# Optimization experiments

Hardware: AMD Instinct MI355X
Metric: run time of the kernel (lower is better)

Reference implementation:

```python
import jax, jax.numpy as jnp
import numpy as np

EPS = 1e-5
H = 6  # num_heads

def batchnorm(x, g, b):
    # BatchNorm1d over node dim using batch statistics (biased var, eps=1e-5)
    mu = x.mean(0)
    var = jnp.mean((x - mu) ** 2, 0)
    return (x - mu) * jax.lax.rsqrt(var + EPS) * g + b

def setup_inputs() -> dict:
    key = jax.random.key(0)
    ks = jax.random.split(key, 16)
    N, E, D = 20000, 200000, 384
    DH = 2 * D  # mlp hidden = dim * mlp_ratio(2.0)
    s = 0.05
    lin = lambda k, i, o: jax.random.normal(k, (i, o), jnp.float32) * s
    inp = {}
    inp['x'] = jax.random.normal(ks[0], (N, D), jnp.float32)
    inp['edge_index'] = jax.random.randint(ks[1], (2, E), 0, N)
    inp['edge_attr'] = jax.random.normal(ks[2], (E, D), jnp.float32)
    # norm1
    inp['g1'] = jnp.ones((D,), jnp.float32); inp['b1'] = jnp.zeros((D,), jnp.float32)
    # TransformerConv-style attention (concat=True, beta=False, edge_dim=D)
    inp['Wq'] = lin(ks[3], D, D); inp['bq'] = jnp.zeros((D,), jnp.float32)
    inp['Wk'] = lin(ks[4], D, D); inp['bk'] = jnp.zeros((D,), jnp.float32)
    inp['Wv'] = lin(ks[5], D, D); inp['bv'] = jnp.zeros((D,), jnp.float32)
    inp['We'] = lin(ks[6], D, D)  # lin_edge, no bias
    inp['Wskip'] = lin(ks[7], D, D); inp['bskip'] = jnp.zeros((D,), jnp.float32)
    # norm2
    inp['g2'] = jnp.ones((D,), jnp.float32); inp['b2'] = jnp.zeros((D,), jnp.float32)
    # Mlp
    inp['W1'] = lin(ks[8], D, DH); inp['bm1'] = jnp.zeros((DH,), jnp.float32)
    inp['W2'] = lin(ks[9], DH, D); inp['bm2'] = jnp.zeros((D,), jnp.float32)
    return inp

def reference(x, edge_index, edge_attr, g1, b1, Wq, bq, Wk, bk, Wv, bv, We, Wskip, bskip, g2, b2, W1, bm1, W2, bm2):
    N, D = x.shape
    Dh = D // H
    scale = 1.0 / jnp.sqrt(jnp.float32(Dh))
    h = batchnorm(x, g1, b1)
    q = (h @ Wq + bq).reshape(N, H, Dh)
    k = (h @ Wk + bk).reshape(N, H, Dh)
    v = (h @ Wv + bv).reshape(N, H, Dh)
    e = (edge_attr @ We).reshape(-1, H, Dh)  # [E,H,Dh]
    src, dst = edge_index[0], edge_index[1]
    ke = k[src] + e  # edge attr added to key
    ve = v[src] + e  # and to value (PyG TransformerConv)
    logits = jnp.einsum('ehd,ehd->eh', q[dst], ke) * scale  # [E,H]
    # segment softmax over incoming edges of each dst node
    m = jax.ops.segment_max(logits, dst, num_segments=N)
    a = jnp.exp(logits - m[dst])
    ssum = jax.ops.segment_sum(a, dst, num_segments=N)
    denom = ssum[dst]
    a = a / jnp.where(denom == 0, 1.0, denom)
    agg = jax.ops.segment_sum(a[:, :, None] * ve, dst, num_segments=N).reshape(N, D)
    attn = agg + (h @ Wskip + bskip)  # root skip (lin_skip)
    x = x + attn  # residual 1 (drop_path/dropout disabled in eval)
    h2 = batchnorm(x, g2, b2)
    mlp = jax.nn.gelu(h2 @ W1 + bm1, approximate=False) @ W2 + bm2
    return x + mlp
```

## Files before the change

### kernel.cpp

```cpp
#include <hip/hip_runtime.h>
#include <hip/hip_bf16.h>

#define DD 384
#define NH 6
#define DHID 768

typedef __attribute__((ext_vector_type(8))) short bf16x8;
typedef __attribute__((ext_vector_type(4))) float f32x4;

__device__ __forceinline__ void gload_lds16(const void* gsrc, void* ldst) {
  __builtin_amdgcn_global_load_lds((const __attribute__((address_space(1))) void*)gsrc,
                                   (__attribute__((address_space(3))) void*)ldst,
                                   16, 0, 0);
}

__global__ __launch_bounds__(384) void bn_stats_k(const float* __restrict__ x, float* __restrict__ sums,
                                                  float* __restrict__ sq, int N, int rpb) {
  int d = threadIdx.x;
  int r0 = blockIdx.x * rpb;
  int r1 = min(r0 + rpb, N);
  float s = 0.f, ss = 0.f;
  for (int r = r0; r < r1; ++r) {
    float v = x[(size_t)r * DD + d];
    s += v; ss += v * v;
  }
  atomicAdd(&sums[d], s);
  atomicAdd(&sq[d], ss);
}

__global__ void bn_finalize_k(const float* sums, const float* sq, const float* g, const float* b,
                              float* a, float* c, int N) {
  int d = blockIdx.x * blockDim.x + threadIdx.x;
  if (d >= DD) return;
  float inv = 1.f / (float)N;
  float mu = sums[d] * inv;
  float var = sq[d] * inv - mu * mu;
  float rs = rsqrtf(var + 1e-5f);
  a[d] = rs * g[d];
  c[d] = b[d] - mu * rs * g[d];
}

union BPack { ushort4 u; __hip_bfloat16 b[4]; };

__global__ void norm_to_bf16_k(const float* __restrict__ x, const float* __restrict__ a,
                               const float* __restrict__ c, __hip_bfloat16* __restrict__ h, int total4) {
  int i = blockIdx.x * blockDim.x + threadIdx.x;
  if (i >= total4) return;
  float4 v = ((const float4*)x)[i];
  int d0 = (i * 4) % DD;
  float4 av = *(const float4*)(a + d0);
  float4 cv = *(const float4*)(c + d0);
  BPack p;
  p.b[0] = __float2bfloat16(v.x * av.x + cv.x);
  p.b[1] = __float2bfloat16(v.y * av.y + cv.y);
  p.b[2] = __float2bfloat16(v.z * av.z + cv.z);
  p.b[3] = __float2bfloat16(v.w * av.w + cv.w);
  ((ushort4*)h)[i] = p.u;
}

__global__ void f32_to_bf16_k(const float* __restrict__ in, __hip_bfloat16* __restrict__ out, int total4) {
  int i = blockIdx.x * blockDim.x + threadIdx.x;
  if (i >= total4) return;
  float4 v = ((const float4*)in)[i];
  BPack p;
  p.b[0] = __float2bfloat16(v.x);
  p.b[1] = __float2bfloat16(v.y);
  p.b[2] = __float2bfloat16(v.z);
  p.b[3] = __float2bfloat16(v.w);
  ((ushort4*)out)[i] = p.u;
}

__global__ void transpose_bf16_k(const float* __restrict__ in, __hip_bfloat16* __restrict__ out,
                                 int K, int Nout) {
  int i = blockIdx.x * blockDim.x + threadIdx.x;
  if (i >= K * Nout) return;
  int k = i / Nout, n = i % Nout;
  out[(size_t)n * K + k] = __float2bfloat16(in[i]);
}

__global__ void concat_bias_k(const float* bq, const float* bk, const float* bv, const float* bs,
                              float* out) {
  int i = blockIdx.x * blockDim.x + threadIdx.x;
  if (i >= 1536) return;
  float v = (i < 384) ? bq[i] : (i < 768) ? bk[i - 384] : (i < 1152) ? bv[i - 768] : bs[i - 1152];
  out[i] = v;
}

__global__ void add3_k(const float* __restrict__ x, const float* __restrict__ agg,
                       const float* __restrict__ skip, float* __restrict__ x1, int total4) {
  int i = blockIdx.x * blockDim.x + threadIdx.x;
  if (i >= total4) return;
  float4 a = ((const float4*)x)[i];
  float4 b = ((const float4*)agg)[i];
  float4 c = ((const float4*)skip)[i];
  float4 o;
  o.x = a.x + b.x + c.x; o.y = a.y + b.y + c.y;
  o.z = a.z + b.z + c.z; o.w = a.w + b.w + c.w;
  ((float4*)x1)[i] = o;
}

__global__ void hist_k(const int* __restrict__ ei, int* __restrict__ deg, int E) {
  int i = blockIdx.x * blockDim.x + threadIdx.x;
  if (i < E) atomicAdd(&deg[ei[E + i]], 1);
}

__global__ __launch_bounds__(1024) void scan_k(const int* __restrict__ deg, int* __restrict__ row_start,
                                               int* __restrict__ cursor, int N) {
  __shared__ int part[1024];
  int t = threadIdx.x;
  int ch = (N + 1023) / 1024;
  int c0 = t * ch, c1 = min(c0 + ch, N);
  int s = 0;
  for (int i = c0; i < c1; ++i) s += deg[i];
  part[t] = s;
  __syncthreads();
  for (int off = 1; off < 1024; off <<= 1) {
    int v = (t >= off) ? part[t - off] : 0;
    __syncthreads();
    part[t] += v;
    __syncthreads();
  }
  int run = part[t] - s;
  for (int i = c0; i < c1; ++i) {
    row_start[i] = run; cursor[i] = run; run += deg[i];
  }
  if (t == 1023) row_start[N] = part[1023];
}

__global__ void scatter_k(const int* __restrict__ ei, int* __restrict__ cursor,
                          int* __restrict__ csr_src, int* __restrict__ csr_eid, int E) {
  int i = blockIdx.x * blockDim.x + threadIdx.x;
  if (i >= E) return;
  int s = ei[i], d = ei[E + i];
  int pos = atomicAdd(&cursor[d], 1);
  csr_src[pos] = s;
  csr_eid[pos] = i;
}

__global__ __launch_bounds__(256) void attn_k(const __hip_bfloat16* __restrict__ qkv,
                                              const __hip_bfloat16* __restrict__ ebuf,
                                              const int* __restrict__ row_start,
                                              const int* __restrict__ csr_src,
                                              const int* __restrict__ csr_eid,
                                              float* __restrict__ agg, int N) {
  int wid = (blockIdx.x * blockDim.x + threadIdx.x) >> 6;
  int lane = threadIdx.x & 63;
  if (wid >= N) return;
  float q[NH], acc[NH], psum[NH];
#pragma unroll
  for (int h = 0; h < NH; ++h) {
    q[h] = __bfloat162float(qkv[(size_t)wid * 1152 + h * 64 + lane]);
    acc[h] = 0.f; psum[h] = 0.f;
  }
  int i0 = row_start[wid], i1 = row_start[wid + 1];
  for (int i = i0; i < i1; ++i) {
    int s = csr_src[i];
    size_t eb = (size_t)csr_eid[i] * DD;
    size_t sb = (size_t)s * 1152;
    float ev[NH], p[NH];
#pragma unroll
    for (int h = 0; h < NH; ++h)
      ev[h] = __bfloat162float(ebuf[eb + h * 64 + lane]);
#pragma unroll
    for (int h = 0; h < NH; ++h) {
      float kk = __bfloat162float(qkv[sb + 384 + h * 64 + lane]);
      float t = q[h] * (kk + ev[h]);
#pragma unroll
      for (int off = 32; off > 0; off >>= 1) t += __shfl_xor(t, off);
      p[h] = expf(t * 0.125f);
    }
#pragma unroll
    for (int h = 0; h < NH; ++h) {
      float vv = __bfloat162float(qkv[sb + 768 + h * 64 + lane]) + ev[h];
      acc[h] += p[h] * vv;
      psum[h] += p[h];
    }
  }
#pragma unroll
  for (int h = 0; h < NH; ++h)
    agg[(size_t)wid * DD + h * 64 + lane] = psum[h] > 0.f ? acc[h] / psum[h] : 0.f;
}

#define BM 128
#define BN 128
#define BK 32

enum { M_QKVS = 0, M_BF16 = 1, M_GELU = 2, M_RES = 3 };

template <int MODE>
__global__ __launch_bounds__(256) void gemm_k(const __hip_bfloat16* __restrict__ A,
                                              const __hip_bfloat16* __restrict__ BT,
                                              const float* __restrict__ bias,
                                              const float* __restrict__ res,
                                              void* __restrict__ out0, void* __restrict__ out1,
                                              int M, int K, int Nn) {
  __shared__ short lA[BM * BK];
  __shared__ short lB[BN * BK];
  int t = threadIdx.x;
  int lane = t & 63, w = t >> 6;
  int wr = (w >> 1) * 64, wc = (w & 1) * 64;
  int row0 = blockIdx.x * BM, col0 = blockIdx.y * BN;
  int lr = lane & 15, lk = lane >> 4;
  f32x4 acc[4][4] = {};

  for (int kt = 0; kt < K; kt += BK) {
    __syncthreads();
#pragma unroll
    for (int j = 0; j < 2; ++j) {
      int chunk = j * 256 + t;
      int r = chunk >> 2, kc = chunk & 3;
      int wavebase = (j * 256 + w * 64) * 8;
      int gra = row0 + r; gra = gra < M ? gra : M - 1;
      gload_lds16(A + (size_t)gra * K + kt + kc * 8, &lA[wavebase]);
      int grb = col0 + r;
      gload_lds16(BT + (size_t)grb * K + kt + kc * 8, &lB[wavebase]);
    }
    __syncthreads();
    bf16x8 af[4], bfr[4];
#pragma unroll
    for (int mi = 0; mi < 4; ++mi)
      af[mi] = *(const bf16x8*)&lA[(wr + mi * 16 + lr) * BK + lk * 8];
#pragma unroll
    for (int ni = 0; ni < 4; ++ni)
      bfr[ni] = *(const bf16x8*)&lB[(wc + ni * 16 + lr) * BK + lk * 8];
#pragma unroll
    for (int mi = 0; mi < 4; ++mi)
#pragma unroll
      for (int ni = 0; ni < 4; ++ni)
        acc[mi][ni] = __builtin_amdgcn_mfma_f32_16x16x32_bf16(af[mi], bfr[ni], acc[mi][ni], 0, 0, 0);
  }

#pragma unroll
  for (int mi = 0; mi < 4; ++mi) {
#pragma unroll
    for (int r = 0; r < 4; ++r) {
      int row = row0 + wr + mi * 16 + lk * 4 + r;
      if (row >= M) continue;
#pragma unroll
      for (int ni = 0; ni < 4; ++ni) {
        int col = col0 + wc + ni * 16 + lr;
        float v = acc[mi][ni][r];
        if constexpr (MODE == M_QKVS) {
          v += bias[col];
          if (col < 1152)
            ((__hip_bfloat16*)out0)[(size_t)row * 1152 + col] = __float2bfloat16(v);
          else
            ((float*)out1)[(size_t)row * DD + (col - 1152)] = v;
        } else if constexpr (MODE == M_BF16) {
          ((__hip_bfloat16*)out0)[(size_t)row * Nn + col] = __float2bfloat16(v);
        } else if constexpr (MODE == M_GELU) {
          v += bias[col];
          v = 0.5f * v * (1.f + erff(v * 0.70710678118f));
          ((__hip_bfloat16*)out0)[(size_t)row * Nn + col] = __float2bfloat16(v);
        } else {
          v += bias[col];
          ((float*)out0)[(size_t)row * Nn + col] = v + res[(size_t)row * Nn + col];
        }
      }
    }
  }
}

extern "C" void kernel_launch(void* const* d_in, const int* in_sizes, int n_in,
                              void* d_out, int out_size, void* d_ws, size_t ws_size,
                              hipStream_t stream) {
  const float* x   = (const float*)d_in[0];
  const int*   ei  = (const int*)d_in[1];
  const float* ea  = (const float*)d_in[2];
  const float* g1  = (const float*)d_in[3];
  const float* b1  = (const float*)d_in[4];
  const float* Wq  = (const float*)d_in[5];
  const float* bq  = (const float*)d_in[6];
  const float* Wk  = (const float*)d_in[7];
  const float* bk  = (const float*)d_in[8];
  const float* Wv  = (const float*)d_in[9];
  const float* bv  = (const float*)d_in[10];
  const float* We  = (const float*)d_in[11];
  const float* Wsk = (const float*)d_in[12];
  const float* bsk = (const float*)d_in[13];
  const float* g2  = (const float*)d_in[14];
  const float* b2  = (const float*)d_in[15];
  const float* W1  = (const float*)d_in[16];
  const float* bm1 = (const float*)d_in[17];
  const float* W2  = (const float*)d_in[18];
  const float* bm2 = (const float*)d_in[19];

  int N = in_sizes[0] / DD;
  int E = in_sizes[1] / 2;

  char* ws = (char*)d_ws;
  size_t off = 0;
  auto alloc = [&](size_t bytes) -> char* {
    char* p = ws + off;
    off = (off + bytes + 255) & ~(size_t)255;
    return p;
  };

  float* bnsum = (float*)alloc(4 * DD * sizeof(float));
  float* a1 = (float*)alloc(DD * 4);
  float* c1 = (float*)alloc(DD * 4);
  float* a2 = (float*)alloc(DD * 4);
  float* c2 = (float*)alloc(DD * 4);
  float* bqkvs = (float*)alloc(1536 * 4);
  __hip_bfloat16* WqkvsT = (__hip_bfloat16*)alloc((size_t)1536 * DD * 2);
  __hip_bfloat16* WeT = (__hip_bfloat16*)alloc((size_t)DD * DD * 2);
  __hip_bfloat16* W1T = (__hip_bfloat16*)alloc((size_t)DHID * DD * 2);
  __hip_bfloat16* W2T = (__hip_bfloat16*)alloc((size_t)DD * DHID * 2);
  __hip_bfloat16* hbuf = (__hip_bfloat16*)alloc((size_t)N * DD * 2);
  __hip_bfloat16* qkv = (__hip_bfloat16*)alloc((size_t)N * 1152 * 2);
  float* skip = (float*)alloc((size_t)N * DD * 4);
  __hip_bfloat16* eabf = (__hip_bfloat16*)alloc((size_t)E * DD * 2);
  __hip_bfloat16* ebuf = (__hip_bfloat16*)alloc((size_t)E * DD * 2);
  float* agg = (float*)alloc((size_t)N * DD * 4);
  float* x1 = (float*)alloc((size_t)N * DD * 4);
  int* deg = (int*)alloc((size_t)N * 4);
  int* cursor = (int*)alloc((size_t)N * 4);
  int* row_start = (int*)alloc((size_t)(N + 1) * 4);
  int* csr_src = (int*)alloc((size_t)E * 4);
  int* csr_eid = (int*)alloc((size_t)E * 4);
  __hip_bfloat16* hid = eabf;
  (void)ws_size; (void)n_in; (void)out_size;

  hipMemsetAsync(bnsum, 0, 4 * DD * sizeof(float), stream);
  hipMemsetAsync(deg, 0, (size_t)N * 4, stream);

  int rpb = 128, sgrid = (N + rpb - 1) / rpb;
  bn_stats_k<<<sgrid, DD, 0, stream>>>(x, bnsum, bnsum + DD, N, rpb);
  bn_finalize_k<<<2, 256, 0, stream>>>(bnsum, bnsum + DD, g1, b1, a1, c1, N);

  int t4 = N * DD / 4;
  norm_to_bf16_k<<<(t4 + 255) / 256, 256, 0, stream>>>(x, a1, c1, hbuf, t4);

  int wgrid = (DD * DD + 255) / 256;
  transpose_bf16_k<<<wgrid, 256, 0, stream>>>(Wq, WqkvsT, DD, DD);
  transpose_bf16_k<<<wgrid, 256, 0, stream>>>(Wk, WqkvsT + (size_t)DD * DD, DD, DD);
  transpose_bf16_k<<<wgrid, 256, 0, stream>>>(Wv, WqkvsT + (size_t)2 * DD * DD, DD, DD);
  transpose_bf16_k<<<wgrid, 256, 0, stream>>>(Wsk, WqkvsT + (size_t)3 * DD * DD, DD, DD);
  transpose_bf16_k<<<wgrid, 256, 0, stream>>>(We, WeT, DD, DD);
  transpose_bf16_k<<<(DD * DHID + 255) / 256, 256, 0, stream>>>(W1, W1T, DD, DHID);
  transpose_bf16_k<<<(DHID * DD + 255) / 256, 256, 0, stream>>>(W2, W2T, DHID, DD);
  concat_bias_k<<<6, 256, 0, stream>>>(bq, bk, bv, bsk, bqkvs);

  int e4 = E * DD / 4;
  f32_to_bf16_k<<<(e4 + 255) / 256, 256, 0, stream>>>(ea, eabf, e4);

  dim3 gqkvs((N + BM - 1) / BM, 1536 / BN);
  gemm_k<M_QKVS><<<gqkvs, 256, 0, stream>>>(hbuf, WqkvsT, bqkvs, nullptr, qkv, skip, N, DD, 1536);

  dim3 ge((E + BM - 1) / BM, DD / BN);
  gemm_k<M_BF16><<<ge, 256, 0, stream>>>(eabf, WeT, nullptr, nullptr, ebuf, nullptr, E, DD, DD);

  hist_k<<<(E + 255) / 256, 256, 0, stream>>>(ei, deg, E);
  scan_k<<<1, 1024, 0, stream>>>(deg, row_start, cursor, N);
  scatter_k<<<(E + 255) / 256, 256, 0, stream>>>(ei, cursor, csr_src, csr_eid, E);

  attn_k<<<(N * 64 + 255) / 256, 256, 0, stream>>>(qkv, ebuf, row_start, csr_src, csr_eid, agg, N);

  add3_k<<<(t4 + 255) / 256, 256, 0, stream>>>(x, agg, skip, x1, t4);

  bn_stats_k<<<sgrid, DD, 0, stream>>>(x1, bnsum + 2 * DD, bnsum + 3 * DD, N, rpb);
  bn_finalize_k<<<2, 256, 0, stream>>>(bnsum + 2 * DD, bnsum + 3 * DD, g2, b2, a2, c2, N);
  norm_to_bf16_k<<<(t4 + 255) / 256, 256, 0, stream>>>(x1, a2, c2, hbuf, t4);

  dim3 gm1((N + BM - 1) / BM, DHID / BN);
  gemm_k<M_GELU><<<gm1, 256, 0, stream>>>(hbuf, W1T, bm1, nullptr, hid, nullptr, N, DD, DHID);

  dim3 gm2((N + BM - 1) / BM, DD / BN);
  gemm_k<M_RES><<<gm2, 256, 0, stream>>>(hid, W2T, bm2, x1, (float*)d_out, nullptr, N, DHID, DD);
}
```

Before: 684.4 us.

## Fold BatchNorm into GEMM weights, convert fp32 inputs in-GEMM, fuse residual with stats

The BatchNorm scale is folded into the transposed weights, and its shift becomes a bias term computed as bias + c·W. The GEMMs then read raw fp32 activations (x, edge_attr, x1) and convert them to bf16 while staging into LDS, so the separate normalize and convert kernels and their bf16 intermediates go away. The residual add is fused with the second BN statistics pass, and GEMM workgroups are remapped so neighbouring tiles land on the same XCD. In exchange, A tiles now come through register-path fp32 loads instead of direct global-to-LDS loads, which doubles A read bytes per tile. Applying the BN scale to weights before rounding to bf16 also changes rounding slightly.

Result: slower. 1.057 ms (+54.5%).

```diff
diff --git a/kernel.cpp b/kernel.cpp
--- a/kernel.cpp
+++ b/kernel.cpp
@@ -12,6 +12,13 @@
   __builtin_amdgcn_global_load_lds((const __attribute__((address_space(1))) void*)gsrc,
                                    (__attribute__((address_space(3))) void*)ldst,
                                    16, 0, 0);
+}
+
+__device__ __forceinline__ short f2bf(float x) {
+  __hip_bfloat16 h = __float2bfloat16(x);
+  union { __hip_bfloat16 h; short s; } u;
+  u.h = h;
+  return u.s;
 }
 
 __global__ __launch_bounds__(384) void bn_stats_k(const float* __restrict__ x, float* __restrict__ sums,
@@ -40,63 +47,41 @@
   c[d] = b[d] - mu * rs * g[d];
 }
 
-union BPack { ushort4 u; __hip_bfloat16 b[4]; };
-
-__global__ void norm_to_bf16_k(const float* __restrict__ x, const float* __restrict__ a,
-                               const float* __restrict__ c, __hip_bfloat16* __restrict__ h, int total4) {
-  int i = blockIdx.x * blockDim.x + threadIdx.x;
-  if (i >= total4) return;
-  float4 v = ((const float4*)x)[i];
-  int d0 = (i * 4) % DD;
-  float4 av = *(const float4*)(a + d0);
-  float4 cv = *(const float4*)(c + d0);
-  BPack p;
-  p.b[0] = __float2bfloat16(v.x * av.x + cv.x);
-  p.b[1] = __float2bfloat16(v.y * av.y + cv.y);
-  p.b[2] = __float2bfloat16(v.z * av.z + cv.z);
-  p.b[3] = __float2bfloat16(v.w * av.w + cv.w);
-  ((ushort4*)h)[i] = p.u;
-}
-
-__global__ void f32_to_bf16_k(const float* __restrict__ in, __hip_bfloat16* __restrict__ out, int total4) {
-  int i = blockIdx.x * blockDim.x + threadIdx.x;
-  if (i >= total4) return;
-  float4 v = ((const float4*)in)[i];
-  BPack p;
-  p.b[0] = __float2bfloat16(v.x);
-  p.b[1] = __float2bfloat16(v.y);
-  p.b[2] = __float2bfloat16(v.z);
-  p.b[3] = __float2bfloat16(v.w);
-  ((ushort4*)out)[i] = p.u;
-}
-
-__global__ void transpose_bf16_k(const float* __restrict__ in, __hip_bfloat16* __restrict__ out,
-                                 int K, int Nout) {
+__global__ void transpose_scale_k(const float* __restrict__ in, const float* __restrict__ a,
+                                  __hip_bfloat16* __restrict__ out, int K, int Nout) {
   int i = blockIdx.x * blockDim.x + threadIdx.x;
   if (i >= K * Nout) return;
   int k = i / Nout, n = i % Nout;
-  out[(size_t)n * K + k] = __float2bfloat16(in[i]);
-}
-
-__global__ void concat_bias_k(const float* bq, const float* bk, const float* bv, const float* bs,
-                              float* out) {
-  int i = blockIdx.x * blockDim.x + threadIdx.x;
-  if (i >= 1536) return;
-  float v = (i < 384) ? bq[i] : (i < 768) ? bk[i - 384] : (i < 1152) ? bv[i - 768] : bs[i - 1152];
-  out[i] = v;
-}
-
-__global__ void add3_k(const float* __restrict__ x, const float* __restrict__ agg,
-                       const float* __restrict__ skip, float* __restrict__ x1, int total4) {
-  int i = blockIdx.x * blockDim.x + threadIdx.x;
-  if (i >= total4) return;
-  float4 a = ((const float4*)x)[i];
-  float4 b = ((const float4*)agg)[i];
-  float4 c = ((const float4*)skip)[i];
-  float4 o;
-  o.x = a.x + b.x + c.x; o.y = a.y + b.y + c.y;
-  o.z = a.z + b.z + c.z; o.w = a.w + b.w + c.w;
-  ((float4*)x1)[i] = o;
+  float v = in[i];
+  if (a) v *= a[k];
+  out[(size_t)n * K + k] = __float2bfloat16(v);
+}
+
+__global__ void bias_cw_k(const float* __restrict__ bias, const float* __restrict__ c,
+                          const float* __restrict__ W, float* __restrict__ out, int K, int Nn) {
+  int n = blockIdx.x * blockDim.x + threadIdx.x;
+  if (n >= Nn) return;
+  float s = bias ? bias[n] : 0.f;
+  for (int k = 0; k < K; ++k) s += c[k] * W[(size_t)k * Nn + n];
+  out[n] = s;
+}
+
+__global__ __launch_bounds__(384) void add3_bn_k(const float* __restrict__ x, const float* __restrict__ agg,
+                                                 const float* __restrict__ skip, float* __restrict__ x1,
+                                                 float* __restrict__ sums, float* __restrict__ sq,
+                                                 int N, int rpb) {
+  int d = threadIdx.x;
+  int r0 = blockIdx.x * rpb;
+  int r1 = min(r0 + rpb, N);
+  float s = 0.f, ss = 0.f;
+  for (int r = r0; r < r1; ++r) {
+    size_t i = (size_t)r * DD + d;
+    float v = x[i] + agg[i] + skip[i];
+    x1[i] = v;
+    s += v; ss += v * v;
+  }
+  atomicAdd(&sums[d], s);
+  atomicAdd(&sq[d], ss);
 }
 
 __global__ void hist_k(const int* __restrict__ ei, int* __restrict__ deg, int E) {
@@ -187,19 +172,26 @@
 
 enum { M_QKVS = 0, M_BF16 = 1, M_GELU = 2, M_RES = 3 };
 
-template <int MODE>
-__global__ __launch_bounds__(256) void gemm_k(const __hip_bfloat16* __restrict__ A,
+template <int MODE, int AF32>
+__global__ __launch_bounds__(256) void gemm_k(const void* __restrict__ Aab,
                                               const __hip_bfloat16* __restrict__ BT,
                                               const float* __restrict__ bias,
                                               const float* __restrict__ res,
                                               void* __restrict__ out0, void* __restrict__ out1,
-                                              int M, int K, int Nn) {
+                                              int M, int K, int Nn, int tn) {
   __shared__ short lA[BM * BK];
   __shared__ short lB[BN * BK];
   int t = threadIdx.x;
   int lane = t & 63, w = t >> 6;
   int wr = (w >> 1) * 64, wc = (w & 1) * 64;
-  int row0 = blockIdx.x * BM, col0 = blockIdx.y * BN;
+
+  int nwg = gridDim.x, bid = blockIdx.x;
+  int q8 = nwg >> 3, r8 = nwg & 7;
+  int xcd = bid & 7, lid = bid >> 3;
+  int wgid = (xcd < r8 ? xcd * (q8 + 1) : r8 * (q8 + 1) + (xcd - r8) * q8) + lid;
+  int bx = wgid / tn, by = wgid % tn;
+  int row0 = bx * BM, col0 = by * BN;
+
   int lr = lane & 15, lk = lane >> 4;
   f32x4 acc[4][4] = {};
 
@@ -208,12 +200,32 @@
 #pragma unroll
     for (int j = 0; j < 2; ++j) {
       int chunk = j * 256 + t;
-      int r = chunk >> 2, kc = chunk & 3;
+      int rB = chunk >> 2, kc = chunk & 3;
       int wavebase = (j * 256 + w * 64) * 8;
-      int gra = row0 + r; gra = gra < M ? gra : M - 1;
-      gload_lds16(A + (size_t)gra * K + kt + kc * 8, &lA[wavebase]);
-      int grb = col0 + r;
-      gload_lds16(BT + (size_t)grb * K + kt + kc * 8, &lB[wavebase]);
+      gload_lds16(BT + (size_t)(col0 + rB) * K + kt + kc * 8, &lB[wavebase]);
+    }
+    if constexpr (AF32) {
+      int rA = t >> 1, half = t & 1;
+      int gra = row0 + rA; gra = gra < M ? gra : M - 1;
+      const float4* ap = (const float4*)((const float*)Aab + (size_t)gra * K + kt + half * 16);
+      float4 f0 = ap[0], f1 = ap[1], f2 = ap[2], f3 = ap[3];
+      bf16x8 v0, v1;
+      v0[0] = f2bf(f0.x); v0[1] = f2bf(f0.y); v0[2] = f2bf(f0.z); v0[3] = f2bf(f0.w);
+      v0[4] = f2bf(f1.x); v0[5] = f2bf(f1.y); v0[6] = f2bf(f1.z); v0[7] = f2bf(f1.w);
+      v1[0] = f2bf(f2.x); v1[1] = f2bf(f2.y); v1[2] = f2bf(f2.z); v1[3] = f2bf(f2.w);
+      v1[4] = f2bf(f3.x); v1[5] = f2bf(f3.y); v1[6] = f2bf(f3.z); v1[7] = f2bf(f3.w);
+      *(__shared__ bf16x8*)&lA[rA * BK + half * 16] = v0;
+      *(__shared__ bf16x8*)&lA[rA * BK + half * 16 + 8] = v1;
+    } else {
+      const __hip_bfloat16* A = (const __hip_bfloat16*)Aab;
+#pragma unroll
+      for (int j = 0; j < 2; ++j) {
+        int chunk = j * 256 + t;
+        int rA = chunk >> 2, kc = chunk & 3;
+        int wavebase = (j * 256 + w * 64) * 8;
+        int gra = row0 + rA; gra = gra < M ? gra : M - 1;
+        gload_lds16(A + (size_t)gra * K + kt + kc * 8, &lA[wavebase]);
+      }
     }
     __syncthreads();
     bf16x8 af[4], bfr[4];
@@ -302,69 +314,64 @@
   float* a2 = (float*)alloc(DD * 4);
   float* c2 = (float*)alloc(DD * 4);
   float* bqkvs = (float*)alloc(1536 * 4);
+  float* bm1p = (float*)alloc(DHID * 4);
   __hip_bfloat16* WqkvsT = (__hip_bfloat16*)alloc((size_t)1536 * DD * 2);
   __hip_bfloat16* WeT = (__hip_bfloat16*)alloc((size_t)DD * DD * 2);
   __hip_bfloat16* W1T = (__hip_bfloat16*)alloc((size_t)DHID * DD * 2);
   __hip_bfloat16* W2T = (__hip_bfloat16*)alloc((size_t)DD * DHID * 2);
-  __hip_bfloat16* hbuf = (__hip_bfloat16*)alloc((size_t)N * DD * 2);
   __hip_bfloat16* qkv = (__hip_bfloat16*)alloc((size_t)N * 1152 * 2);
   float* skip = (float*)alloc((size_t)N * DD * 4);
-  __hip_bfloat16* eabf = (__hip_bfloat16*)alloc((size_t)E * DD * 2);
   __hip_bfloat16* ebuf = (__hip_bfloat16*)alloc((size_t)E * DD * 2);
   float* agg = (float*)alloc((size_t)N * DD * 4);
   float* x1 = (float*)alloc((size_t)N * DD * 4);
+  __hip_bfloat16* hid = (__hip_bfloat16*)alloc((size_t)N * DHID * 2);
   int* deg = (int*)alloc((size_t)N * 4);
   int* cursor = (int*)alloc((size_t)N * 4);
   int* row_start = (int*)alloc((size_t)(N + 1) * 4);
   int* csr_src = (int*)alloc((size_t)E * 4);
   int* csr_eid = (int*)alloc((size_t)E * 4);
-  __hip_bfloat16* hid = eabf;
   (void)ws_size; (void)n_in; (void)out_size;
 
   hipMemsetAsync(bnsum, 0, 4 * DD * sizeof(float), stream);
   hipMemsetAsync(deg, 0, (size_t)N * 4, stream);
+
+  hist_k<<<(E + 255) / 256, 256, 0, stream>>>(ei, deg, E);
+  scan_k<<<1, 1024, 0, stream>>>(deg, row_start, cursor, N);
+  scatter_k<<<(E + 255) / 256, 256, 0, stream>>>(ei, cursor, csr_src, csr_eid, E);
 
   int rpb = 128, sgrid = (N + rpb - 1) / rpb;
   bn_stats_k<<<sgrid, DD, 0, stream>>>(x, bnsum, bnsum + DD, N, rpb);
   bn_finalize_k<<<2, 256, 0, stream>>>(bnsum, bnsum + DD, g1, b1, a1, c1, N);
 
-  int t4 = N * DD / 4;
-  norm_to_bf16_k<<<(t4 + 255) / 256, 256, 0, stream>>>(x, a1, c1, hbuf, t4);
-
   int wgrid = (DD * DD + 255) / 256;
-  transpose_bf16_k<<<wgrid, 256, 0, stream>>>(Wq, WqkvsT, DD, DD);
-  transpose_bf16_k<<<wgrid, 256, 0, stream>>>(Wk, WqkvsT + (size_t)DD * DD, DD, DD);
-  transpose_bf16_k<<<wgrid, 256, 0, stream>>>(Wv, WqkvsT + (size_t)2 * DD * DD, DD, DD);
-  transpose_bf16_k<<<wgrid, 256, 0, stream>>>(Wsk, WqkvsT + (size_t)3 * DD * DD, DD, DD);
-  transpose_bf16_k<<<wgrid, 256, 0, stream>>>(We, WeT, DD, DD);
-  transpose_bf16_k<<<(DD * DHID + 255) / 256, 256, 0, stream>>>(W1, W1T, DD, DHID);
-  transpose_bf16_k<<<(DHID * DD + 255) / 256, 256, 0, stream>>>(W2, W2T, DHID, DD);
-  concat_bias_k<<<6, 256, 0, stream>>>(bq, bk, bv, bsk, bqkvs);
-
-  int e4 = E * DD / 4;
-  f32_to_bf16_k<<<(e4 + 255) / 256, 256, 0, stream>>>(ea, eabf, e4);
-
-  dim3 gqkvs((N + BM - 1) / BM, 1536 / BN);
-  gemm_k<M_QKVS><<<gqkvs, 256, 0, stream>>>(hbuf, WqkvsT, bqkvs, nullptr, qkv, skip, N, DD, 1536);
-
-  dim3 ge((E + BM - 1) / BM, DD / BN);
-  gemm_k<M_BF16><<<ge, 256, 0, stream>>>(eabf, WeT, nullptr, nullptr, ebuf, nullptr, E, DD, DD);
-
-  hist_k<<<(E + 255) / 256, 256, 0, stream>>>(ei, deg, E);
-  scan_k<<<1, 1024, 0, stream>>>(deg, row_start, cursor, N);
-  scatter_k<<<(E + 255) / 256, 256, 0, stream>>>(ei, cursor, csr_src, csr_eid, E);
+  transpose_scale_k<<<wgrid, 256, 0, stream>>>(Wq, a1, WqkvsT, DD, DD);
+  transpose_scale_k<<<wgrid, 256, 0, stream>>>(Wk, a1, WqkvsT + (size_t)DD * DD, DD, DD);
+  transpose_scale_k<<<wgrid, 256, 0, stream>>>(Wv, a1, WqkvsT + (size_t)2 * DD * DD, DD, DD);
+  transpose_scale_k<<<wgrid, 256, 0, stream>>>(Wsk, a1, WqkvsT + (size_t)3 * DD * DD, DD, DD);
+  transpose_scale_k<<<wgrid, 256, 0, stream>>>(We, nullptr, WeT, DD, DD);
+  transpose_scale_k<<<(DHID * DD + 255) / 256, 256, 0, stream>>>(W2, nullptr, W2T, DHID, DD);
+  bias_cw_k<<<2, 256, 0, stream>>>(bq, c1, Wq, bqkvs, DD, DD);
+  bias_cw_k<<<2, 256, 0, stream>>>(bk, c1, Wk, bqkvs + DD, DD, DD);
+  bias_cw_k<<<2, 256, 0, stream>>>(bv, c1, Wv, bqkvs + 2 * DD, DD, DD);
+  bias_cw_k<<<2, 256, 0, stream>>>(bsk, c1, Wsk, bqkvs + 3 * DD, DD, DD);
+
+  dim3 gqkvs((N + BM - 1) / BM * (1536 / BN));
+  gemm_k<M_QKVS, 1><<<gqkvs, 256, 0, stream>>>(x, WqkvsT, bqkvs, nullptr, qkv, skip, N, DD, 1536, 1536 / BN);
+
+  dim3 ge((E + BM - 1) / BM * (DD / BN));
+  gemm_k<M_BF16, 1><<<ge, 256, 0, stream>>>(ea, WeT, nullptr, nullptr, ebuf, nullptr, E, DD, DD, DD / BN);
 
   attn_k<<<(N * 64 + 255) / 256, 256, 0, stream>>>(qkv, ebuf, row_start, csr_src, csr_eid, agg, N);
 
-  add3_k<<<(t4 + 255) / 256, 256, 0, stream>>>(x, agg, skip, x1, t4);
-
-  bn_stats_k<<<sgrid, DD, 0, stream>>>(x1, bnsum + 2 * DD, bnsum + 3 * DD, N, rpb);
+  add3_bn_k<<<sgrid, DD, 0, stream>>>(x, agg, skip, x1, bnsum + 2 * DD, bnsum + 3 * DD, N, rpb);
   bn_finalize_k<<<2, 256, 0, stream>>>(bnsum + 2 * DD, bnsum + 3 * DD, g2, b2, a2, c2, N);
-  norm_to_bf16_k<<<(t4 + 255) / 256, 256, 0, stream>>>(x1, a2, c2, hbuf, t4);
-
-  dim3 gm1((N + BM - 1) / BM, DHID / BN);
-  gemm_k<M_GELU><<<gm1, 256, 0, stream>>>(hbuf, W1T, bm1, nullptr, hid, nullptr, N, DD, DHID);
-
-  dim3 gm2((N + BM - 1) / BM, DD / BN);
-  gemm_k<M_RES><<<gm2, 256, 0, stream>>>(hid, W2T, bm2, x1, (float*)d_out, nullptr, N, DHID, DD);
-}
+
+  transpose_scale_k<<<(DD * DHID + 255) / 256, 256, 0, stream>>>(W1, a2, W1T, DD, DHID);
+  bias_cw_k<<<3, 256, 0, stream>>>(bm1, c2, W1, bm1p, DD, DHID);
+
+  dim3 gm1((N + BM - 1) / BM * (DHID / BN));
+  gemm_k<M_GELU, 1><<<gm1, 256, 0, stream>>>(x1, W1T, bm1p, nullptr, hid, nullptr, N, DD, DHID, DHID / BN);
+
+  dim3 gm2((N + BM - 1) / BM * (DD / BN));
+  gemm_k<M_RES, 0><<<gm2, 256, 0, stream>>>(hid, W2T, bm2, x1, (float*)d_out, nullptr, N, DHID, DD, DD / BN);
+}
```

## Process four edges per wavefront in attention kernel with vectorized bf16 loads

Applied to the files above, without the earlier changes.

Each 64-lane wavefront now splits into four 16-lane groups that each handle a different incoming edge. Each lane loads four bf16 values at a time, which shortens the dot-product shuffle reduction from six steps to four. Partial accumulators are combined across the groups at the end, and the output is written as float4. This removes the one-edge-at-a-time serialization and the scalar 2-byte loads, at the cost of more registers and idle lanes when a node's in-degree is not a multiple of four. It also switches to the fast __expf intrinsic. There is still no max subtraction in the softmax, as before.

New measurement: 688.4 us. Within noise of the previous version (+0.6%).

```diff
diff --git a/kernel.cpp b/kernel.cpp
--- a/kernel.cpp
+++ b/kernel.cpp
@@ -12,6 +12,12 @@
   __builtin_amdgcn_global_load_lds((const __attribute__((address_space(1))) void*)gsrc,
                                    (__attribute__((address_space(3))) void*)ldst,
                                    16, 0, 0);
+}
+
+__device__ __forceinline__ float b2f(unsigned short u) {
+  union { unsigned int i; float f; } c;
+  c.i = (unsigned int)u << 16;
+  return c.f;
 }
 
 __global__ __launch_bounds__(384) void bn_stats_k(const float* __restrict__ x, float* __restrict__ sums,
@@ -146,39 +152,71 @@
   int wid = (blockIdx.x * blockDim.x + threadIdx.x) >> 6;
   int lane = threadIdx.x & 63;
   if (wid >= N) return;
-  float q[NH], acc[NH], psum[NH];
+  int g = lane >> 4, l = lane & 15;
+  const ushort* qk = (const ushort*)qkv;
+  const ushort* eu = (const ushort*)ebuf;
+  float q[NH][4], acc[NH][4], psum[NH];
 #pragma unroll
   for (int h = 0; h < NH; ++h) {
-    q[h] = __bfloat162float(qkv[(size_t)wid * 1152 + h * 64 + lane]);
-    acc[h] = 0.f; psum[h] = 0.f;
+    ushort4 u = *(const ushort4*)&qk[(size_t)wid * 1152 + h * 64 + l * 4];
+    q[h][0] = b2f(u.x); q[h][1] = b2f(u.y); q[h][2] = b2f(u.z); q[h][3] = b2f(u.w);
+#pragma unroll
+    for (int j = 0; j < 4; ++j) acc[h][j] = 0.f;
+    psum[h] = 0.f;
   }
   int i0 = row_start[wid], i1 = row_start[wid + 1];
-  for (int i = i0; i < i1; ++i) {
-    int s = csr_src[i];
-    size_t eb = (size_t)csr_eid[i] * DD;
-    size_t sb = (size_t)s * 1152;
-    float ev[NH], p[NH];
-#pragma unroll
-    for (int h = 0; h < NH; ++h)
-      ev[h] = __bfloat162float(ebuf[eb + h * 64 + lane]);
+  for (int i = i0; i < i1; i += 4) {
+    int e = i + g;
+    bool valid = e < i1;
+    int ec = valid ? e : i1 - 1;
+    size_t sb = (size_t)csr_src[ec] * 1152;
+    size_t eb = (size_t)csr_eid[ec] * 384;
+    float ev[NH][4], p[NH];
 #pragma unroll
     for (int h = 0; h < NH; ++h) {
-      float kk = __bfloat162float(qkv[sb + 384 + h * 64 + lane]);
-      float t = q[h] * (kk + ev[h]);
-#pragma unroll
-      for (int off = 32; off > 0; off >>= 1) t += __shfl_xor(t, off);
-      p[h] = expf(t * 0.125f);
+      ushort4 ue = *(const ushort4*)&eu[eb + h * 64 + l * 4];
+      ev[h][0] = b2f(ue.x); ev[h][1] = b2f(ue.y); ev[h][2] = b2f(ue.z); ev[h][3] = b2f(ue.w);
+      ushort4 uk = *(const ushort4*)&qk[sb + 384 + h * 64 + l * 4];
+      float t = q[h][0] * (b2f(uk.x) + ev[h][0]);
+      t += q[h][1] * (b2f(uk.y) + ev[h][1]);
+      t += q[h][2] * (b2f(uk.z) + ev[h][2]);
+      t += q[h][3] * (b2f(uk.w) + ev[h][3]);
+      t += __shfl_xor(t, 1);
+      t += __shfl_xor(t, 2);
+      t += __shfl_xor(t, 4);
+      t += __shfl_xor(t, 8);
+      p[h] = valid ? __expf(t * 0.125f) : 0.f;
     }
 #pragma unroll
     for (int h = 0; h < NH; ++h) {
-      float vv = __bfloat162float(qkv[sb + 768 + h * 64 + lane]) + ev[h];
-      acc[h] += p[h] * vv;
+      ushort4 uv = *(const ushort4*)&qk[sb + 768 + h * 64 + l * 4];
+      acc[h][0] += p[h] * (b2f(uv.x) + ev[h][0]);
+      acc[h][1] += p[h] * (b2f(uv.y) + ev[h][1]);
+      acc[h][2] += p[h] * (b2f(uv.z) + ev[h][2]);
+      acc[h][3] += p[h] * (b2f(uv.w) + ev[h][3]);
       psum[h] += p[h];
     }
   }
 #pragma unroll
-  for (int h = 0; h < NH; ++h)
-    agg[(size_t)wid * DD + h * 64 + lane] = psum[h] > 0.f ? acc[h] / psum[h] : 0.f;
+  for (int h = 0; h < NH; ++h) {
+#pragma unroll
+    for (int j = 0; j < 4; ++j) {
+      acc[h][j] += __shfl_xor(acc[h][j], 16);
+      acc[h][j] += __shfl_xor(acc[h][j], 32);
+    }
+    psum[h] += __shfl_xor(psum[h], 16);
+    psum[h] += __shfl_xor(psum[h], 32);
+  }
+  if (lane < 16) {
+#pragma unroll
+    for (int h = 0; h < NH; ++h) {
+      float inv = psum[h] > 0.f ? 1.f / psum[h] : 0.f;
+      float4 o;
+      o.x = acc[h][0] * inv; o.y = acc[h][1] * inv;
+      o.z = acc[h][2] * inv; o.w = acc[h][3] * inv;
+      *(float4*)&agg[(size_t)wid * DD + h * 64 + l * 4] = o;
+    }
+  }
 }
 
 #define BM 128
```
